# Performance work log

Hardware: AMD Instinct MI355X
Metric: run time of the kernel (lower is better)

## Reference

```python
import jax, jax.numpy as jnp
import numpy as np

H = 256          # hidden_size
V_IN = 29        # in_embeddng_size
V_OUT = 74       # out_embedding_size
L = 32           # encoder sequence length
STEPS = 20       # max_decoding_steps
BOS, EOS = 2, 3


def gru_cell(x, h, Wih, Whh, bih, bhh):
    # torch GRU cell: r,z,n gate order in the stacked [3H, H] weight matrices
    gi = x @ Wih.T + bih          # [3H]
    gh = h @ Whh.T + bhh          # [3H]
    ir, iz, inn = jnp.split(gi, 3)
    hr, hz, hn = jnp.split(gh, 3)
    r = jax.nn.sigmoid(ir + hr)
    z = jax.nn.sigmoid(iz + hz)
    n = jnp.tanh(inn + r * hn)
    return (1.0 - z) * n + z * h


def setup_inputs() -> dict:
    key = jax.random.key(0)
    ks = jax.random.split(key, 14)
    f = lambda k, shape: (jax.random.normal(k, shape, jnp.float32) * 0.08)
    inp = {
        "enc_input": jax.random.randint(ks[0], (1, L), 0, V_IN).astype(jnp.int32),
        "enc_emb": f(ks[1], (V_IN, H)).at[0].set(0.0),   # padding_idx=0
        "enc_Wih": f(ks[2], (3 * H, H)),
        "enc_Whh": f(ks[3], (3 * H, H)),
        "enc_bih": f(ks[4], (3 * H,)),
        "enc_bhh": f(ks[5], (3 * H,)),
        "dec_emb": f(ks[6], (V_OUT, H)).at[0].set(0.0),  # padding_idx=0
        "dec_Wih": f(ks[7], (3 * H, H)),
        "dec_Whh": f(ks[8], (3 * H, H)),
        "dec_bih": f(ks[9], (3 * H,)),
        "dec_bhh": f(ks[10], (3 * H,)),
        "fc_W": f(ks[11], (V_OUT, H)),
        "fc_b": f(ks[12], (V_OUT,)),
    }
    return inp


def reference(enc_input, enc_emb, enc_Wih, enc_Whh, enc_bih, enc_bhh,
              dec_emb, dec_Wih, dec_Whh, dec_bih, dec_bhh, fc_W, fc_b):
    # ---- encoder: embed + single-layer GRU over the sequence (batch=1) ----
    x_seq = enc_emb[enc_input[0]]                     # [L, H]
    def enc_step(h, x):
        return gru_cell(x, h, enc_Wih, enc_Whh, enc_bih, enc_bhh), None
    h0 = jnp.zeros((H,), enc_emb.dtype)
    h, _ = jax.lax.scan(enc_step, h0, x_seq)          # final hidden [H]

    # Early break is emulated by a `done` flag: once EOS is emitted, all
    # subsequent preds stay 0 (matching torch, which leaves preds zeros).
    def dec_step(carry, _):
        h, tok, done = carry
        x = dec_emb[tok]
        h2 = gru_cell(x, h, dec_Wih, dec_Whh, dec_bih, dec_bhh)
        logit = h2 @ fc_W.T + fc_b                    # [V_OUT]
        topi = jnp.argmax(logit).astype(jnp.int32)    # topk(1) == argmax
        is_eos = topi == EOS
        pred = jnp.where(done | is_eos, 0, topi)      # EOS step not recorded
        return (h2, topi, done | is_eos), pred

    init = (h, jnp.int32(BOS), jnp.bool_(False))
    _, preds = jax.lax.scan(dec_step, init, None, length=STEPS)
    return preds                                      # [20] int32
```

## Files before the change

### kernel.cpp

```cpp
#include <hip/hip_runtime.h>
#include <cmath>

#define H     256
#define H3    768
#define L     32
#define STEPS 20
#define VOUT  74
#define NP    16
#define NB    128
#define HW    16
#define ROWS  48
#define NITEMS (L + VOUT)

#define WS_CNT   0
#define WS_WIN   8
#define WS_HX    16
#define WS_EGI   1040
#define WS_DGI   (1040 + NP * L * ROWS)

__device__ __forceinline__ float sigmoidf_(float x) {
    return 1.0f / (1.0f + expf(-x));
}

__device__ __forceinline__ int growf(int w, int lr) {
    int j = w * HW + (lr & 15);
    return (lr < 16) ? j : (lr < 32 ? H + j : 2 * H + j);
}

__global__ void prep(const int*   __restrict__ enc_input,
                     const float* __restrict__ enc_emb,
                     const float* __restrict__ encWih,
                     const float* __restrict__ enc_bih,
                     const float* __restrict__ dec_emb,
                     const float* __restrict__ decWih,
                     const float* __restrict__ dec_bih,
                     float* __restrict__ ws) {
    if (blockIdx.x == 0) {
        for (int k = threadIdx.x; k < 1040; k += 256) ((int*)ws)[k] = 0;
        if (threadIdx.x == 0) ((int*)ws)[WS_WIN] = -1;
    }
    int wid  = blockIdx.x * 4 + (threadIdx.x >> 6);
    int lane = threadIdx.x & 63;
    if (wid >= NITEMS * H3) return;
    int item = wid / H3;
    int j    = wid - item * H3;
    int wOwn = (j & 255) >> 4;
    int lr   = (j >> 8) * 16 + (j & 15);

    const float* x; const float* W; const float* b; float* out;
    if (item < L) {
        x = enc_emb + enc_input[item] * H;  W = encWih + j * H;
        b = enc_bih;
        out = ws + WS_EGI + (wOwn * L + item) * ROWS + lr;
    } else {
        int v = item - L;
        x = dec_emb + v * H;                W = decWih + j * H;
        b = dec_bih;
        out = ws + WS_DGI + (wOwn * VOUT + v) * ROWS + lr;
    }
    float4 w  = ((const float4*)W)[lane];
    float4 xv = ((const float4*)x)[lane];
    float s = fmaf(w.x, xv.x, fmaf(w.y, xv.y, fmaf(w.z, xv.z, w.w * xv.w)));
    #pragma unroll
    for (int m = 1; m < 64; m <<= 1) s += __shfl_xor(s, m);
    if (lane == 0) *out = s + b[j];
}

__global__ __launch_bounds__(256, 1) void gru_seq(
        const float* __restrict__ enc_Whh, const float* __restrict__ enc_bhh,
        const float* __restrict__ dec_Whh, const float* __restrict__ dec_bhh,
        const float* __restrict__ fc_W,    const float* __restrict__ fc_b,
        float* __restrict__ ws, int* __restrict__ out) {
    __shared__ __align__(16) float hl[1040];
    __shared__ float fb[VOUT];
    __shared__ float gh_l[ROWS];
    __shared__ float egi_l[L * ROWS];
    __shared__ float dgi_l[VOUT * ROWS];
    __shared__ float log_l[VOUT];
    __shared__ int   s_tok, s_done, s_role;

    const int t = threadIdx.x;

    if (t == 0) {
        int xcd;
        asm volatile("s_getreg_b32 %0, hwreg(HW_REG_XCC_ID)" : "=s"(xcd));
        xcd &= 7;
        int* cnt = (int*)ws + WS_CNT;
        int* win = (int*)ws + WS_WIN;
        int rank = __hip_atomic_fetch_add(&cnt[xcd], 1, __ATOMIC_RELAXED,
                                          __HIP_MEMORY_SCOPE_AGENT);
        if (rank == NP - 1) {
            int expect = -1;
            __hip_atomic_compare_exchange_strong(win, &expect, xcd,
                __ATOMIC_RELAXED, __ATOMIC_RELAXED, __HIP_MEMORY_SCOPE_AGENT);
        }
        int wv;
        while ((wv = __hip_atomic_load(win, __ATOMIC_RELAXED,
                                       __HIP_MEMORY_SCOPE_AGENT)) < 0)
            __builtin_amdgcn_s_sleep(2);
        s_role = (wv == xcd && rank < NP) ? rank : -1;
        s_done = 0; s_tok = 2;
    }
    __syncthreads();
    const int w = s_role;
    if (w < 0) return;

    unsigned long long* hx = (unsigned long long*)((int*)ws + WS_HX);

    if (w == 0 && t < STEPS) out[t] = 0;
    if (t < VOUT) fb[t] = fc_b[t];
    for (int idx = t; idx < L * ROWS; idx += 256)
        egi_l[idx] = ws[WS_EGI + w * (L * ROWS) + idx];
    for (int idx = t; idx < VOUT * ROWS; idx += 256)
        dgi_l[idx] = ws[WS_DGI + w * (VOUT * ROWS) + idx];

    const int m  = t - 64;
    const int p  = t & 3;
    const int lr = (t >= 64) ? (m >> 2) : 0;
    const int g  = growf(w, lr);
    float4 wE[16], wD[16];
    float bhhE = 0.f, bhhD = 0.f;
    if (t >= 64) {
        const float* eb = enc_Whh + g * H + p * 64;
        const float* db = dec_Whh + g * H + p * 64;
        #pragma unroll
        for (int i = 0; i < 16; ++i) {
            wE[i] = *(const float4*)(eb + 4 * i);
            wD[i] = *(const float4*)(db + 4 * i);
        }
        if (p == 0) { bhhE = enc_bhh[g]; bhhD = dec_bhh[g]; }
    }

    const int rF = t >> 2;
    float4 wF[16], wF2[16];
    {
        const float* fp = fc_W + rF * H + p * 64;
        #pragma unroll
        for (int i = 0; i < 16; ++i) wF[i] = *(const float4*)(fp + 4 * i);
        if (t < 40) {
            const float* fp2 = fc_W + (64 + rF) * H + p * 64;
            #pragma unroll
            for (int i = 0; i < 16; ++i) wF2[i] = *(const float4*)(fp2 + 4 * i);
        }
    }

    int tok = 2;
    for (int s = 0; s <= L + STEPS; ++s) {
        {
            const unsigned long long* src = hx + (s & 1) * H + t;
            unsigned long long u = __hip_atomic_load(src, __ATOMIC_RELAXED,
                                                     __HIP_MEMORY_SCOPE_AGENT);
            while ((unsigned)u != (unsigned)s) {
                __builtin_amdgcn_s_sleep(1);
                u = __hip_atomic_load(src, __ATOMIC_RELAXED,
                                      __HIP_MEMORY_SCOPE_AGENT);
            }
            float hv = __uint_as_float((unsigned)(u >> 32));
            hl[t] = hv; hl[260 + t] = hv; hl[520 + t] = hv; hl[780 + t] = hv;
        }
        __syncthreads();

        const bool dec_out = (s >= L + 1);
        if (dec_out) {
            const float* hb = hl + p * 324;
            float a = 0.f;
            #pragma unroll
            for (int i = 0; i < 16; ++i) {
                float4 h4 = *(const float4*)(hb + 4 * i);
                a = fmaf(wF[i].x, h4.x, fmaf(wF[i].y, h4.y,
                      fmaf(wF[i].z, h4.z, fmaf(wF[i].w, h4.w, a))));
            }
            a += __shfl_xor(a, 1); a += __shfl_xor(a, 2);
            if (p == 0) log_l[rF] = a + fb[rF];
            if (t < 40) {
                float a2 = 0.f;
                #pragma unroll
                for (int i = 0; i < 16; ++i) {
                    float4 h4 = *(const float4*)(hb + 4 * i);
                    a2 = fmaf(wF2[i].x, h4.x, fmaf(wF2[i].y, h4.y,
                           fmaf(wF2[i].z, h4.z, fmaf(wF2[i].w, h4.w, a2))));
                }
                a2 += __shfl_xor(a2, 1); a2 += __shfl_xor(a2, 2);
                if (p == 0) log_l[64 + rF] = a2 + fb[64 + rF];
            }
            __syncthreads();
        }

        if (t < 64) {
            if (dec_out) {
                float v = log_l[t]; int bi = t;
                if (t < VOUT - 64) {
                    float v2 = log_l[64 + t];
                    if (v2 > v) { v = v2; bi = 64 + t; }
                }
                #pragma unroll
                for (int mm = 1; mm < 64; mm <<= 1) {
                    float ov = __shfl_xor(v, mm);
                    int   ob = __shfl_xor(bi, mm);
                    if (ov > v || (ov == v && ob < bi)) { v = ov; bi = ob; }
                }
                if (t == 0) {
                    bool eos = (bi == 3);
                    if (w == 0 && !eos) out[s - (L + 1)] = bi;
                    s_tok = bi;
                    if (eos) s_done = 1;
                }
            }
        } else {
            float acc = (s < L) ? bhhE : bhhD;
            const float* hb = hl + p * 324;
            if (s < L) {
                #pragma unroll
                for (int i = 0; i < 16; ++i) {
                    float4 h4 = *(const float4*)(hb + 4 * i);
                    acc = fmaf(wE[i].x, h4.x, fmaf(wE[i].y, h4.y,
                          fmaf(wE[i].z, h4.z, fmaf(wE[i].w, h4.w, acc))));
                }
            } else {
                #pragma unroll
                for (int i = 0; i < 16; ++i) {
                    float4 h4 = *(const float4*)(hb + 4 * i);
                    acc = fmaf(wD[i].x, h4.x, fmaf(wD[i].y, h4.y,
                          fmaf(wD[i].z, h4.z, fmaf(wD[i].w, h4.w, acc))));
                }
            }
            acc += __shfl_xor(acc, 1);
            acc += __shfl_xor(acc, 2);
            if (p == 0) gh_l[m >> 2] = acc;
        }
        __syncthreads();

        if (dec_out) {
            tok = s_tok;
            if (s_done || s == L + STEPS) break;
        }

        if (t < HW) {
            const float* gi = (s < L) ? (egi_l + s * ROWS) : (dgi_l + tok * ROWS);
            float r = sigmoidf_(gi[t]      + gh_l[t]);
            float z = sigmoidf_(gi[16 + t] + gh_l[16 + t]);
            float n = tanhf    (gi[32 + t] + r * gh_l[32 + t]);
            float hn = (1.f - z) * n + z * hl[w * HW + t];
            unsigned long long pk =
                ((unsigned long long)__float_as_uint(hn) << 32) |
                (unsigned)(s + 1);
            __hip_atomic_store(hx + ((s + 1) & 1) * H + w * HW + t, pk,
                               __ATOMIC_RELAXED, __HIP_MEMORY_SCOPE_AGENT);
        }
    }
}

extern "C" void kernel_launch(void* const* d_in, const int* in_sizes, int n_in,
                              void* d_out, int out_size, void* d_ws, size_t ws_size,
                              hipStream_t stream) {
    const int*   enc_input = (const int*)  d_in[0];
    const float* enc_emb   = (const float*)d_in[1];
    const float* enc_Wih   = (const float*)d_in[2];
    const float* enc_Whh   = (const float*)d_in[3];
    const float* enc_bih   = (const float*)d_in[4];
    const float* enc_bhh   = (const float*)d_in[5];
    const float* dec_emb   = (const float*)d_in[6];
    const float* dec_Wih   = (const float*)d_in[7];
    const float* dec_Whh   = (const float*)d_in[8];
    const float* dec_bih   = (const float*)d_in[9];
    const float* dec_bhh   = (const float*)d_in[10];
    const float* fc_W      = (const float*)d_in[11];
    const float* fc_b      = (const float*)d_in[12];
    float* ws  = (float*)d_ws;
    int*  outp = (int*)d_out;

    hipLaunchKernelGGL(prep, dim3((NITEMS * H3 + 3) / 4), dim3(256), 0, stream,
                       enc_input, enc_emb, enc_Wih, enc_bih,
                       dec_emb, dec_Wih, dec_bih, ws);
    hipLaunchKernelGGL(gru_seq, dim3(NB), dim3(256), 0, stream,
                       enc_Whh, enc_bhh, dec_Whh, dec_bhh, fc_W, fc_b,
                       ws, outp);
}
```

Measured before the change: 133.8 us.

## Poll hidden-state handoff via L2 atomics with padded slots and batch prep weights

Replaces the relaxed atomic-load spin on the hidden-state exchange with polling through a zero-add atomic. Published values are now spread into cache-line-padded slots, and a mirrored copy is read through the old load path as a fallback. The prep kernel is restructured so each wavefront loads one weight row once and reuses it across 8 input items, which cuts grid size and redundant weight loads. The dot-product loops are also split into two accumulators to shorten FMA dependency chains. The costs are more atomic traffic to L2 and a larger workspace footprint.

```diff
diff --git a/kernel.cpp b/kernel.cpp
--- a/kernel.cpp
+++ b/kernel.cpp
@@ -10,13 +10,13 @@
 #define NB    128
 #define HW    16
 #define ROWS  48
-#define NITEMS (L + VOUT)
 
 #define WS_CNT   0
 #define WS_WIN   8
-#define WS_HX    16
-#define WS_EGI   1040
-#define WS_DGI   (1040 + NP * L * ROWS)
+#define WS_HD    16
+#define WS_HM    8208
+#define WS_EGI   10256
+#define WS_DGI   (10256 + NP * L * ROWS)
 
 __device__ __forceinline__ float sigmoidf_(float x) {
     return 1.0f / (1.0f + expf(-x));
@@ -25,6 +25,21 @@
 __device__ __forceinline__ int growf(int w, int lr) {
     int j = w * HW + (lr & 15);
     return (lr < 16) ? j : (lr < 32 ? H + j : 2 * H + j);
+}
+
+__device__ __forceinline__ unsigned long long l2_poll(
+        const unsigned long long* p) {
+    unsigned long long old;
+    unsigned long long zero = 0;
+    asm volatile("global_atomic_add_x2 %0, %1, %2, off sc0\n\t"
+                 "s_waitcnt vmcnt(0)"
+                 : "=&v"(old) : "v"(p), "v"(zero) : "memory");
+    return old;
+}
+__device__ __forceinline__ void l2_publish(unsigned long long* p,
+                                           unsigned long long v) {
+    asm volatile("global_atomic_swap_x2 %0, %1, off"
+                 :: "v"(p), "v"(v) : "memory");
 }
 
 __global__ void prep(const int*   __restrict__ enc_input,
@@ -36,34 +51,43 @@
                      const float* __restrict__ dec_bih,
                      float* __restrict__ ws) {
     if (blockIdx.x == 0) {
-        for (int k = threadIdx.x; k < 1040; k += 256) ((int*)ws)[k] = 0;
-        if (threadIdx.x == 0) ((int*)ws)[WS_WIN] = -1;
+        for (int k = threadIdx.x; k < 10256; k += 256)
+            ((int*)ws)[k] = (k == WS_WIN) ? -1 : 0;
     }
     int wid  = blockIdx.x * 4 + (threadIdx.x >> 6);
     int lane = threadIdx.x & 63;
-    if (wid >= NITEMS * H3) return;
-    int item = wid / H3;
-    int j    = wid - item * H3;
+
+    int j, i0, nIt; const float* W; const float* b; bool isEnc;
+    if (wid < 3072) {
+        j = wid >> 2; i0 = (wid & 3) * 8; nIt = 8;
+        W = encWih; b = enc_bih; isEnc = true;
+    } else {
+        int w2 = wid - 3072;
+        if (w2 >= 7680) return;
+        j = w2 / 10; i0 = (w2 % 10) * 8;
+        nIt = (VOUT - i0 < 8) ? (VOUT - i0) : 8;
+        W = decWih; b = dec_bih; isEnc = false;
+    }
+    float4 wv = ((const float4*)(W + j * H))[lane];
+    float bj = b[j];
     int wOwn = (j & 255) >> 4;
     int lr   = (j >> 8) * 16 + (j & 15);
 
-    const float* x; const float* W; const float* b; float* out;
-    if (item < L) {
-        x = enc_emb + enc_input[item] * H;  W = encWih + j * H;
-        b = enc_bih;
-        out = ws + WS_EGI + (wOwn * L + item) * ROWS + lr;
-    } else {
-        int v = item - L;
-        x = dec_emb + v * H;                W = decWih + j * H;
-        b = dec_bih;
-        out = ws + WS_DGI + (wOwn * VOUT + v) * ROWS + lr;
-    }
-    float4 w  = ((const float4*)W)[lane];
-    float4 xv = ((const float4*)x)[lane];
-    float s = fmaf(w.x, xv.x, fmaf(w.y, xv.y, fmaf(w.z, xv.z, w.w * xv.w)));
-    #pragma unroll
-    for (int m = 1; m < 64; m <<= 1) s += __shfl_xor(s, m);
-    if (lane == 0) *out = s + b[j];
+    for (int ii = 0; ii < nIt; ++ii) {
+        int item = i0 + ii;
+        const float* x = isEnc ? (enc_emb + enc_input[item] * H)
+                               : (dec_emb + item * H);
+        float4 xv = ((const float4*)x)[lane];
+        float s = fmaf(wv.x, xv.x, fmaf(wv.y, xv.y, fmaf(wv.z, xv.z, wv.w * xv.w)));
+        #pragma unroll
+        for (int m = 1; m < 64; m <<= 1) s += __shfl_xor(s, m);
+        if (lane == 0) {
+            float* op = isEnc
+                ? ws + WS_EGI + (wOwn * L + item) * ROWS + lr
+                : ws + WS_DGI + (wOwn * VOUT + item) * ROWS + lr;
+            *op = s + bj;
+        }
+    }
 }
 
 __global__ __launch_bounds__(256, 1) void gru_seq(
@@ -105,7 +129,8 @@
     const int w = s_role;
     if (w < 0) return;
 
-    unsigned long long* hx = (unsigned long long*)((int*)ws + WS_HX);
+    unsigned long long* hd = (unsigned long long*)((int*)ws + WS_HD);
+    unsigned long long* hm = (unsigned long long*)((int*)ws + WS_HM);
 
     if (w == 0 && t < STEPS) out[t] = 0;
     if (t < VOUT) fb[t] = fc_b[t];
@@ -147,13 +172,19 @@
     int tok = 2;
     for (int s = 0; s <= L + STEPS; ++s) {
         {
-            const unsigned long long* src = hx + (s & 1) * H + t;
-            unsigned long long u = __hip_atomic_load(src, __ATOMIC_RELAXED,
-                                                     __HIP_MEMORY_SCOPE_AGENT);
+            const unsigned long long* fast = hd + ((s & 1) * H + t) * 8;
+            const unsigned long long* slow = hm + (s & 1) * H + t;
+            unsigned long long u = l2_poll(fast);
+            int spin = 0;
             while ((unsigned)u != (unsigned)s) {
-                __builtin_amdgcn_s_sleep(1);
-                u = __hip_atomic_load(src, __ATOMIC_RELAXED,
-                                      __HIP_MEMORY_SCOPE_AGENT);
+                if (++spin >= 256) {
+                    spin = 0;
+                    u = __hip_atomic_load(slow, __ATOMIC_RELAXED,
+                                          __HIP_MEMORY_SCOPE_AGENT);
+                    if ((unsigned)u == (unsigned)s) break;
+                }
+                __builtin_amdgcn_s_sleep(3);
+                u = l2_poll(fast);
             }
             float hv = __uint_as_float((unsigned)(u >> 32));
             hl[t] = hv; hl[260 + t] = hv; hl[520 + t] = hv; hl[780 + t] = hv;
@@ -163,23 +194,31 @@
         const bool dec_out = (s >= L + 1);
         if (dec_out) {
             const float* hb = hl + p * 324;
-            float a = 0.f;
+            float a0 = 0.f, a1 = 0.f;
             #pragma unroll
-            for (int i = 0; i < 16; ++i) {
-                float4 h4 = *(const float4*)(hb + 4 * i);
-                a = fmaf(wF[i].x, h4.x, fmaf(wF[i].y, h4.y,
-                      fmaf(wF[i].z, h4.z, fmaf(wF[i].w, h4.w, a))));
-            }
+            for (int i = 0; i < 16; i += 2) {
+                float4 h4a = *(const float4*)(hb + 4 * i);
+                float4 h4b = *(const float4*)(hb + 4 * i + 4);
+                a0 = fmaf(wF[i].x, h4a.x, fmaf(wF[i].y, h4a.y,
+                      fmaf(wF[i].z, h4a.z, fmaf(wF[i].w, h4a.w, a0))));
+                a1 = fmaf(wF[i+1].x, h4b.x, fmaf(wF[i+1].y, h4b.y,
+                      fmaf(wF[i+1].z, h4b.z, fmaf(wF[i+1].w, h4b.w, a1))));
+            }
+            float a = a0 + a1;
             a += __shfl_xor(a, 1); a += __shfl_xor(a, 2);
             if (p == 0) log_l[rF] = a + fb[rF];
             if (t < 40) {
-                float a2 = 0.f;
+                float b0 = 0.f, b1 = 0.f;
                 #pragma unroll
-                for (int i = 0; i < 16; ++i) {
-                    float4 h4 = *(const float4*)(hb + 4 * i);
-                    a2 = fmaf(wF2[i].x, h4.x, fmaf(wF2[i].y, h4.y,
-                           fmaf(wF2[i].z, h4.z, fmaf(wF2[i].w, h4.w, a2))));
-                }
+                for (int i = 0; i < 16; i += 2) {
+                    float4 h4a = *(const float4*)(hb + 4 * i);
+                    float4 h4b = *(const float4*)(hb + 4 * i + 4);
+                    b0 = fmaf(wF2[i].x, h4a.x, fmaf(wF2[i].y, h4a.y,
+                          fmaf(wF2[i].z, h4a.z, fmaf(wF2[i].w, h4a.w, b0))));
+                    b1 = fmaf(wF2[i+1].x, h4b.x, fmaf(wF2[i+1].y, h4b.y,
+                          fmaf(wF2[i+1].z, h4b.z, fmaf(wF2[i+1].w, h4b.w, b1))));
+                }
+                float a2 = b0 + b1;
                 a2 += __shfl_xor(a2, 1); a2 += __shfl_xor(a2, 2);
                 if (p == 0) log_l[64 + rF] = a2 + fb[64 + rF];
             }
@@ -207,23 +246,30 @@
                 }
             }
         } else {
-            float acc = (s < L) ? bhhE : bhhD;
+            float acc0 = (s < L) ? bhhE : bhhD, acc1 = 0.f;
             const float* hb = hl + p * 324;
             if (s < L) {
                 #pragma unroll
-                for (int i = 0; i < 16; ++i) {
-                    float4 h4 = *(const float4*)(hb + 4 * i);
-                    acc = fmaf(wE[i].x, h4.x, fmaf(wE[i].y, h4.y,
-                          fmaf(wE[i].z, h4.z, fmaf(wE[i].w, h4.w, acc))));
+                for (int i = 0; i < 16; i += 2) {
+                    float4 h4a = *(const float4*)(hb + 4 * i);
+                    float4 h4b = *(const float4*)(hb + 4 * i + 4);
+                    acc0 = fmaf(wE[i].x, h4a.x, fmaf(wE[i].y, h4a.y,
+                           fmaf(wE[i].z, h4a.z, fmaf(wE[i].w, h4a.w, acc0))));
+                    acc1 = fmaf(wE[i+1].x, h4b.x, fmaf(wE[i+1].y, h4b.y,
+                           fmaf(wE[i+1].z, h4b.z, fmaf(wE[i+1].w, h4b.w, acc1))));
                 }
             } else {
                 #pragma unroll
-                for (int i = 0; i < 16; ++i) {
-                    float4 h4 = *(const float4*)(hb + 4 * i);
-                    acc = fmaf(wD[i].x, h4.x, fmaf(wD[i].y, h4.y,
-                          fmaf(wD[i].z, h4.z, fmaf(wD[i].w, h4.w, acc))));
-                }
-            }
+                for (int i = 0; i < 16; i += 2) {
+                    float4 h4a = *(const float4*)(hb + 4 * i);
+                    float4 h4b = *(const float4*)(hb + 4 * i + 4);
+                    acc0 = fmaf(wD[i].x, h4a.x, fmaf(wD[i].y, h4a.y,
+                           fmaf(wD[i].z, h4a.z, fmaf(wD[i].w, h4a.w, acc0))));
+                    acc1 = fmaf(wD[i+1].x, h4b.x, fmaf(wD[i+1].y, h4b.y,
+                           fmaf(wD[i+1].z, h4b.z, fmaf(wD[i+1].w, h4b.w, acc1))));
+                }
+            }
+            float acc = acc0 + acc1;
             acc += __shfl_xor(acc, 1);
             acc += __shfl_xor(acc, 2);
             if (p == 0) gh_l[m >> 2] = acc;
@@ -244,7 +290,9 @@
             unsigned long long pk =
                 ((unsigned long long)__float_as_uint(hn) << 32) |
                 (unsigned)(s + 1);
-            __hip_atomic_store(hx + ((s + 1) & 1) * H + w * HW + t, pk,
+            int unit = w * HW + t, par1 = (s + 1) & 1;
+            l2_publish(hd + (par1 * H + unit) * 8, pk);
+            __hip_atomic_store(hm + par1 * H + unit, pk,
                                __ATOMIC_RELAXED, __HIP_MEMORY_SCOPE_AGENT);
         }
     }
@@ -269,7 +317,7 @@
     float* ws  = (float*)d_ws;
     int*  outp = (int*)d_out;
 
-    hipLaunchKernelGGL(prep, dim3((NITEMS * H3 + 3) / 4), dim3(256), 0, stream,
+    hipLaunchKernelGGL(prep, dim3(2688), dim3(256), 0, stream,
                        enc_input, enc_emb, enc_Wih, enc_bih,
                        dec_emb, dec_Wih, dec_bih, ws);
     hipLaunchKernelGGL(gru_seq, dim3(NB), dim3(256), 0, stream,
```

Result: slower. 151.0 us (+12.8%).
